# Performance work log

Hardware: AMD Instinct MI355X
Metric: run time of the kernel (lower is better)

Reference implementation:

```python
import jax, jax.numpy as jnp
import numpy as np

N_NODES = 100000
N_EDGES = 1600000
IN_DIM = 128
HID = 128
OUT = 40


def setup_inputs() -> dict:
    key = jax.random.key(0)
    ks = jax.random.split(key, 8)
    x = jax.random.normal(ks[0], (N_NODES, IN_DIM), dtype=jnp.float32)
    edge_index = jax.random.randint(ks[1], (2, N_EDGES), 0, N_NODES, dtype=jnp.int64)
    def glorot(k, fan_in, fan_out):
        s = jnp.sqrt(6.0 / (fan_in + fan_out)).astype(jnp.float32)
        return jax.random.uniform(k, (fan_in, fan_out), jnp.float32, -s, s)
    return {
        "x": x,
        "edge_index": edge_index,
        "W1": glorot(ks[2], IN_DIM, HID), "b1": jnp.zeros((HID,), jnp.float32),
        "W2": glorot(ks[3], HID, HID),    "b2": jnp.zeros((HID,), jnp.float32),
        "W3": glorot(ks[4], HID, HID),    "b3": jnp.zeros((HID,), jnp.float32),
        "Wl": glorot(ks[5], HID, OUT),    "bl": jnp.zeros((OUT,), jnp.float32),
    }


def _gcn_norm(edge_index, num_nodes):
    # PyG GCNConv default: add self-loops, symmetric normalization.
    loops = jnp.arange(num_nodes, dtype=edge_index.dtype)
    src = jnp.concatenate([edge_index[0], loops])
    dst = jnp.concatenate([edge_index[1], loops])
    deg = jax.ops.segment_sum(jnp.ones_like(dst, dtype=jnp.float32), dst,
                              num_segments=num_nodes)
    dis = jnp.where(deg > 0, jax.lax.rsqrt(deg), 0.0)  # deg^{-1/2}
    norm = dis[src] * dis[dst]  # [E+N]
    return src, dst, norm


def _gcn_conv(x, W, b, src, dst, norm, num_nodes):
    h = x @ W                                   # [N, F_out]
    msg = h[src] * norm[:, None]                # gather + scale
    out = jax.ops.segment_sum(msg, dst, num_segments=num_nodes)
    return out + b


def reference(x, edge_index, W1, b1, W2, b2, W3, b3, Wl, bl):
    n = x.shape[0]
    src, dst, norm = _gcn_norm(edge_index, n)
    h = jax.nn.relu(_gcn_conv(x, W1, b1, src, dst, norm, n))
    h = jax.nn.relu(_gcn_conv(h, W2, b2, src, dst, norm, n))
    h = _gcn_conv(h, W3, b3, src, dst, norm, n)
    # dropout p=0.5 is identity in eval mode
    return h @ Wl + bl
```

## Files before the change

kernel.cpp:

```cpp
#include <hip/hip_runtime.h>

typedef __attribute__((ext_vector_type(8))) short sh8;
typedef __attribute__((ext_vector_type(4))) float f4;

__device__ __forceinline__ float bf2f(unsigned short u) {
    union { unsigned int u; float f; } c; c.u = ((unsigned int)u) << 16; return c.f;
}
__device__ __forceinline__ unsigned short f2bf(float f) {
    union { float f; unsigned int u; } c; c.f = f;
    unsigned int x = c.u;
    unsigned int r = (x + 0x7fffu + ((x >> 16) & 1u)) >> 16;
    return (unsigned short)r;
}
__device__ __forceinline__ void bfsplit(float x, short& hi, short& lo) {
    unsigned short h = f2bf(x);
    float r = x - bf2f(h);
    hi = (short)h;
    lo = (short)f2bf(r);
}

__global__ void k_zero_cnt(int* cnt, int N) {
    int i = blockIdx.x * 256 + threadIdx.x;
    if (i < N) cnt[i] = 0;
}

__global__ void k_count(const int* __restrict__ dst, int* __restrict__ cnt, int E, int N) {
    int E4 = E >> 2;
    for (int i = blockIdx.x * 256 + threadIdx.x; i < E4; i += gridDim.x * 256) {
        int4 d = ((const int4*)dst)[i];
        if ((unsigned)d.x < (unsigned)N) atomicAdd(&cnt[d.x], 1);
        if ((unsigned)d.y < (unsigned)N) atomicAdd(&cnt[d.y], 1);
        if ((unsigned)d.z < (unsigned)N) atomicAdd(&cnt[d.z], 1);
        if ((unsigned)d.w < (unsigned)N) atomicAdd(&cnt[d.w], 1);
    }
    if (blockIdx.x == 0) {
        for (int e = (E4 << 2) + threadIdx.x; e < E; e += 256) {
            int d = dst[e];
            if ((unsigned)d < (unsigned)N) atomicAdd(&cnt[d], 1);
        }
    }
}

#define SCAN_B 256
__global__ void k_scan_a(const int* __restrict__ cnt, int* __restrict__ rowptr,
                         int* __restrict__ bsum, float* __restrict__ dis, int N) {
    __shared__ int sh[SCAN_B];
    int t = threadIdx.x, i = blockIdx.x * SCAN_B + t;
    int v = (i < N) ? cnt[i] : 0;
    if (i < N) dis[i] = rsqrtf((float)(v + 1));
    sh[t] = v; __syncthreads();
    for (int off = 1; off < SCAN_B; off <<= 1) {
        int x = (t >= off) ? sh[t - off] : 0;
        __syncthreads();
        sh[t] += x;
        __syncthreads();
    }
    int incl = sh[t];
    if (i < N) rowptr[i] = incl - v;
    if (t == SCAN_B - 1) bsum[blockIdx.x] = incl;
}

__global__ void k_scan_b(int* bsum, int NB) {
    __shared__ int sh[512];
    int t = threadIdx.x;
    int v = (t < NB) ? bsum[t] : 0;
    sh[t] = v; __syncthreads();
    for (int off = 1; off < 512; off <<= 1) {
        int x = (t >= off) ? sh[t - off] : 0;
        __syncthreads();
        sh[t] += x;
        __syncthreads();
    }
    if (t < NB) bsum[t] = sh[t] - v;
}

__global__ void k_scan_c(int* __restrict__ rowptr, int* __restrict__ cursor,
                         const int* __restrict__ bsum, int N) {
    int i = blockIdx.x * 256 + threadIdx.x;
    if (i < N) {
        int r = rowptr[i] + bsum[blockIdx.x];
        rowptr[i] = r;
        cursor[i] = r;
    }
}

__global__ void k_fill(const int* __restrict__ src, const int* __restrict__ dst,
                       int* __restrict__ cursor, int* __restrict__ csrc, int E, int N) {
    int g = blockIdx.x & 7;
    int j = blockIdx.x >> 3;
    int nb = gridDim.x >> 3;
    int lo = (int)((long long)g * N / 8);
    int hi = (int)((long long)(g + 1) * N / 8);
    int E4 = E >> 2;
    for (int i = j * 256 + threadIdx.x; i < E4; i += nb * 256) {
        int4 d4 = ((const int4*)dst)[i];
        int e = i << 2;
        #pragma unroll
        for (int q = 0; q < 4; ++q) {
            int d = (q == 0) ? d4.x : (q == 1) ? d4.y : (q == 2) ? d4.z : d4.w;
            if (d < lo || d >= hi) continue;
            int s = src[e + q];
            if ((unsigned)s >= (unsigned)N) continue;
            int p = atomicAdd(&cursor[d], 1);
            csrc[p] = s;
        }
    }
    if (blockIdx.x == 0) {
        for (int e = (E4 << 2) + threadIdx.x; e < E; e += 256) {
            int d = dst[e];
            int s = src[e];
            if ((unsigned)d >= (unsigned)N || (unsigned)s >= (unsigned)N) continue;
            int p = atomicAdd(&cursor[d], 1);
            csrc[p] = s;
        }
    }
}

__global__ __launch_bounds__(256)
void k_gemm128_a32(const float* __restrict__ X,
                   const float* __restrict__ W,
                   const float* __restrict__ dis,
                   unsigned short* __restrict__ H, int nPairs) {
    int wave = threadIdx.x >> 6;
    int lane = threadIdx.x & 63;
    int ln = lane & 15, quad = lane >> 4;
    int c0 = (wave & 1) * 64;
    int subTile = wave >> 1;

    sh8 bh[4][4], blo[4][4];
    #pragma unroll
    for (int nt = 0; nt < 4; ++nt) {
        int col = c0 + nt * 16 + ln;
        #pragma unroll
        for (int kt = 0; kt < 4; ++kt) {
            int k0 = kt * 32 + quad * 8;
            #pragma unroll
            for (int j = 0; j < 8; ++j) {
                short h, l;
                bfsplit(W[(k0 + j) * 128 + col], h, l);
                bh[nt][kt][j] = h; blo[nt][kt][j] = l;
            }
        }
    }

    for (int p = blockIdx.x; p < nPairs; p += gridDim.x) {
        int nodeBase = p * 32 + subTile * 16;
        const float* xrow = X + (nodeBase + ln) * 128 + quad * 8;
        sh8 ah[4], al[4];
        #pragma unroll
        for (int kt = 0; kt < 4; ++kt) {
            f4 v0 = *(const f4*)(xrow + kt * 32);
            f4 v1 = *(const f4*)(xrow + kt * 32 + 4);
            #pragma unroll
            for (int j = 0; j < 4; ++j) {
                short h, l;
                bfsplit(v0[j], h, l); ah[kt][j] = h; al[kt][j] = l;
                bfsplit(v1[j], h, l); ah[kt][j + 4] = h; al[kt][j + 4] = l;
            }
        }

        f4 acc[4] = { {0.f,0.f,0.f,0.f}, {0.f,0.f,0.f,0.f}, {0.f,0.f,0.f,0.f}, {0.f,0.f,0.f,0.f} };
        #pragma unroll
        for (int kt = 0; kt < 4; ++kt)
            #pragma unroll
            for (int nt = 0; nt < 4; ++nt) {
                acc[nt] = __builtin_amdgcn_mfma_f32_16x16x32_bf16(ah[kt], bh[nt][kt], acc[nt], 0, 0, 0);
                acc[nt] = __builtin_amdgcn_mfma_f32_16x16x32_bf16(ah[kt], blo[nt][kt], acc[nt], 0, 0, 0);
                acc[nt] = __builtin_amdgcn_mfma_f32_16x16x32_bf16(al[kt], bh[nt][kt], acc[nt], 0, 0, 0);
            }

        float ds[4];
        #pragma unroll
        for (int r = 0; r < 4; ++r) ds[r] = dis[nodeBase + quad * 4 + r];
        #pragma unroll
        for (int nt = 0; nt < 4; ++nt) {
            int col = c0 + nt * 16 + ln;
            #pragma unroll
            for (int r = 0; r < 4; ++r)
                H[(nodeBase + quad * 4 + r) * 128 + col] = f2bf(acc[nt][r] * ds[r]);
        }
    }
}

__global__ __launch_bounds__(256)
void k_gemm128_a16(const unsigned short* __restrict__ X,
                   const float* __restrict__ W,
                   const float* __restrict__ dis,
                   unsigned short* __restrict__ H, int nPairs) {
    int wave = threadIdx.x >> 6;
    int lane = threadIdx.x & 63;
    int ln = lane & 15, quad = lane >> 4;
    int c0 = (wave & 1) * 64;
    int subTile = wave >> 1;

    sh8 bh[4][4], blo[4][4];
    #pragma unroll
    for (int nt = 0; nt < 4; ++nt) {
        int col = c0 + nt * 16 + ln;
        #pragma unroll
        for (int kt = 0; kt < 4; ++kt) {
            int k0 = kt * 32 + quad * 8;
            #pragma unroll
            for (int j = 0; j < 8; ++j) {
                short h, l;
                bfsplit(W[(k0 + j) * 128 + col], h, l);
                bh[nt][kt][j] = h; blo[nt][kt][j] = l;
            }
        }
    }

    for (int p = blockIdx.x; p < nPairs; p += gridDim.x) {
        int nodeBase = p * 32 + subTile * 16;
        const unsigned short* xrow = X + (nodeBase + ln) * 128 + quad * 8;
        sh8 a[4];
        #pragma unroll
        for (int kt = 0; kt < 4; ++kt) a[kt] = *(const sh8*)(xrow + kt * 32);

        f4 acc[4] = { {0.f,0.f,0.f,0.f}, {0.f,0.f,0.f,0.f}, {0.f,0.f,0.f,0.f}, {0.f,0.f,0.f,0.f} };
        #pragma unroll
        for (int kt = 0; kt < 4; ++kt)
            #pragma unroll
            for (int nt = 0; nt < 4; ++nt) {
                acc[nt] = __builtin_amdgcn_mfma_f32_16x16x32_bf16(a[kt], bh[nt][kt], acc[nt], 0, 0, 0);
                acc[nt] = __builtin_amdgcn_mfma_f32_16x16x32_bf16(a[kt], blo[nt][kt], acc[nt], 0, 0, 0);
            }

        float ds[4];
        #pragma unroll
        for (int r = 0; r < 4; ++r) ds[r] = dis[nodeBase + quad * 4 + r];
        #pragma unroll
        for (int nt = 0; nt < 4; ++nt) {
            int col = c0 + nt * 16 + ln;
            #pragma unroll
            for (int r = 0; r < 4; ++r)
                H[(nodeBase + quad * 4 + r) * 128 + col] = f2bf(acc[nt][r] * ds[r]);
        }
    }
}

__global__ __launch_bounds__(256)
void k_agg(const unsigned short* __restrict__ H,
           unsigned short* __restrict__ O,
           const float* __restrict__ dis,
           const int* __restrict__ rowptr,
           const int* __restrict__ cnt,
           const int* __restrict__ csrc,
           const float* __restrict__ bias,
           int relu, int N) {
    int n = (blockIdx.x * 256 + threadIdx.x) >> 5;
    if (n >= N) return;
    int lane = threadIdx.x & 31;
    int sub  = lane & 15;
    int half = lane >> 4;

    float a0 = 0.f, a1 = 0.f, a2 = 0.f, a3 = 0.f;
    float a4 = 0.f, a5 = 0.f, a6 = 0.f, a7 = 0.f;

    auto addrow = [&](uint4 v) {
        a0 += bf2f((unsigned short)v.x);
        a1 += bf2f((unsigned short)(v.x >> 16));
        a2 += bf2f((unsigned short)v.y);
        a3 += bf2f((unsigned short)(v.y >> 16));
        a4 += bf2f((unsigned short)v.z);
        a5 += bf2f((unsigned short)(v.z >> 16));
        a6 += bf2f((unsigned short)v.w);
        a7 += bf2f((unsigned short)(v.w >> 16));
    };

    if (half == 0)
        addrow(*(const uint4*)(H + (size_t)n * 128 + sub * 8));

    int start = rowptr[n];
    int e = cnt[n];
    int i = 0;
    for (; i + 8 <= e; i += 8) {
        int s[4];
        #pragma unroll
        for (int q = 0; q < 4; ++q) s[q] = csrc[start + i + 2 * q + half];
        uint4 v[4];
        #pragma unroll
        for (int q = 0; q < 4; ++q) v[q] = *(const uint4*)(H + (size_t)s[q] * 128 + sub * 8);
        #pragma unroll
        for (int q = 0; q < 4; ++q) addrow(v[q]);
    }
    for (int j = i + half; j < e; j += 2) {
        int s = csrc[start + j];
        addrow(*(const uint4*)(H + (size_t)s * 128 + sub * 8));
    }

    a0 += __shfl_xor(a0, 16); a1 += __shfl_xor(a1, 16);
    a2 += __shfl_xor(a2, 16); a3 += __shfl_xor(a3, 16);
    a4 += __shfl_xor(a4, 16); a5 += __shfl_xor(a5, 16);
    a6 += __shfl_xor(a6, 16); a7 += __shfl_xor(a7, 16);

    if (half == 0) {
        float dn = dis[n];
        f4 b0 = *(const f4*)(bias + sub * 8);
        f4 b1 = *(const f4*)(bias + sub * 8 + 4);
        a0 = a0 * dn + b0[0]; a1 = a1 * dn + b0[1];
        a2 = a2 * dn + b0[2]; a3 = a3 * dn + b0[3];
        a4 = a4 * dn + b1[0]; a5 = a5 * dn + b1[1];
        a6 = a6 * dn + b1[2]; a7 = a7 * dn + b1[3];
        if (relu) {
            a0 = fmaxf(a0, 0.f); a1 = fmaxf(a1, 0.f);
            a2 = fmaxf(a2, 0.f); a3 = fmaxf(a3, 0.f);
            a4 = fmaxf(a4, 0.f); a5 = fmaxf(a5, 0.f);
            a6 = fmaxf(a6, 0.f); a7 = fmaxf(a7, 0.f);
        }
        uint4 ov;
        ov.x = (unsigned int)f2bf(a0) | ((unsigned int)f2bf(a1) << 16);
        ov.y = (unsigned int)f2bf(a2) | ((unsigned int)f2bf(a3) << 16);
        ov.z = (unsigned int)f2bf(a4) | ((unsigned int)f2bf(a5) << 16);
        ov.w = (unsigned int)f2bf(a6) | ((unsigned int)f2bf(a7) << 16);
        *(uint4*)(O + (size_t)n * 128 + sub * 8) = ov;
    }
}

__global__ __launch_bounds__(256)
void k_gemm_final(const unsigned short* __restrict__ X,
                  const float* __restrict__ W,
                  const float* __restrict__ bl,
                  float* __restrict__ OUT, int nTiles) {
    int wave = threadIdx.x >> 6;
    int lane = threadIdx.x & 63;
    int ln = lane & 15, quad = lane >> 4;
    int tile = blockIdx.x * 4 + wave;
    if (tile >= nTiles) return;

    sh8 bh[3][4], blo[3][4];
    #pragma unroll
    for (int nt = 0; nt < 3; ++nt) {
        int col = nt * 16 + ln;
        bool valid = (col < 40);
        #pragma unroll
        for (int kt = 0; kt < 4; ++kt) {
            int k0 = kt * 32 + quad * 8;
            #pragma unroll
            for (int j = 0; j < 8; ++j) {
                short h = 0, l = 0;
                if (valid) bfsplit(W[(k0 + j) * 40 + col], h, l);
                bh[nt][kt][j] = h; blo[nt][kt][j] = l;
            }
        }
    }

    int nodeBase = tile * 16;
    const unsigned short* xrow = X + (nodeBase + ln) * 128 + quad * 8;
    sh8 a[4];
    #pragma unroll
    for (int kt = 0; kt < 4; ++kt) a[kt] = *(const sh8*)(xrow + kt * 32);

    f4 acc[3] = { {0.f,0.f,0.f,0.f}, {0.f,0.f,0.f,0.f}, {0.f,0.f,0.f,0.f} };
    #pragma unroll
    for (int kt = 0; kt < 4; ++kt)
        #pragma unroll
        for (int nt = 0; nt < 3; ++nt) {
            acc[nt] = __builtin_amdgcn_mfma_f32_16x16x32_bf16(a[kt], bh[nt][kt], acc[nt], 0, 0, 0);
            acc[nt] = __builtin_amdgcn_mfma_f32_16x16x32_bf16(a[kt], blo[nt][kt], acc[nt], 0, 0, 0);
        }

    #pragma unroll
    for (int nt = 0; nt < 3; ++nt) {
        int col = nt * 16 + ln;
        if (col < 40) {
            float bv = bl[col];
            #pragma unroll
            for (int r = 0; r < 4; ++r)
                OUT[(nodeBase + quad * 4 + r) * 40 + col] = acc[nt][r] + bv;
        }
    }
}

extern "C" void kernel_launch(void* const* d_in, const int* in_sizes, int n_in,
                              void* d_out, int out_size, void* d_ws, size_t ws_size,
                              hipStream_t stream) {
    const float* x  = (const float*)d_in[0];
    const int*   ei = (const int*)d_in[1];
    const float* W1 = (const float*)d_in[2];
    const float* b1 = (const float*)d_in[3];
    const float* W2 = (const float*)d_in[4];
    const float* b2 = (const float*)d_in[5];
    const float* W3 = (const float*)d_in[6];
    const float* b3 = (const float*)d_in[7];
    const float* Wl = (const float*)d_in[8];
    const float* bl = (const float*)d_in[9];

    const int N = in_sizes[0] / 128;
    const int E = in_sizes[1] / 2;
    const int* srcIdx = ei;
    const int* dstIdx = ei + E;

    char* ws = (char*)d_ws;
    size_t off = 0;
    auto alloc = [&](size_t bytes) { void* p = ws + off; off += (bytes + 511) & ~(size_t)511; return p; };
    int*   cnt     = (int*)  alloc((size_t)N * 4);
    int*   rowptr  = (int*)  alloc((size_t)N * 4);
    int*   cursor  = (int*)  alloc((size_t)N * 4);
    float* dis     = (float*)alloc((size_t)N * 4);
    int*   bsum    = (int*)  alloc(512 * 4);
    int*   csrc    = (int*)  alloc((size_t)E * 4);
    unsigned short* h0 = (unsigned short*)alloc((size_t)N * 128 * 2);
    unsigned short* h1 = (unsigned short*)alloc((size_t)N * 128 * 2);

    const int gN = (N + 255) / 256;
    const int nPairs = N / 32;
    const int nTiles = N / 16;
    const int gAgg = (N * 32 + 255) / 256;
    const int gPart = 2048;

    k_zero_cnt<<<gN, 256, 0, stream>>>(cnt, N);
    k_count<<<1568, 256, 0, stream>>>(dstIdx, cnt, E, N);
    k_scan_a<<<gN, 256, 0, stream>>>(cnt, rowptr, bsum, dis, N);
    k_scan_b<<<1, 512, 0, stream>>>(bsum, gN);
    k_scan_c<<<gN, 256, 0, stream>>>(rowptr, cursor, bsum, N);
    k_fill<<<gPart, 256, 0, stream>>>(srcIdx, dstIdx, cursor, csrc, E, N);

    k_gemm128_a32<<<768, 256, 0, stream>>>(x, W1, dis, h0, nPairs);
    k_agg<<<gAgg, 256, 0, stream>>>(h0, h1, dis, rowptr, cnt, csrc, b1, 1, N);
    k_gemm128_a16<<<768, 256, 0, stream>>>(h1, W2, dis, h0, nPairs);
    k_agg<<<gAgg, 256, 0, stream>>>(h0, h1, dis, rowptr, cnt, csrc, b2, 1, N);
    k_gemm128_a16<<<768, 256, 0, stream>>>(h1, W3, dis, h0, nPairs);
    k_agg<<<gAgg, 256, 0, stream>>>(h0, h1, dis, rowptr, cnt, csrc, b3, 0, N);
    k_gemm_final<<<(nTiles + 3) / 4, 256, 0, stream>>>(h1, Wl, bl, (float*)d_out, nTiles);
}
```

Before: 539.1 us.

## Store hidden features in 16-wide feature panels and aggregate per panel

```diff
diff --git a/kernel.cpp b/kernel.cpp
--- a/kernel.cpp
+++ b/kernel.cpp
@@ -2,6 +2,7 @@
 
 typedef __attribute__((ext_vector_type(8))) short sh8;
 typedef __attribute__((ext_vector_type(4))) float f4;
+typedef __attribute__((ext_vector_type(4))) unsigned int u4;
 
 __device__ __forceinline__ float bf2f(unsigned short u) {
     union { unsigned int u; float f; } c; c.u = ((unsigned int)u) << 16; return c.f;
@@ -18,6 +19,7 @@
     hi = (short)h;
     lo = (short)f2bf(r);
 }
+
 
 __global__ void k_zero_cnt(int* cnt, int N) {
     int i = blockIdx.x * 256 + threadIdx.x;
@@ -126,6 +128,7 @@
     int ln = lane & 15, quad = lane >> 4;
     int c0 = (wave & 1) * 64;
     int subTile = wave >> 1;
+    const size_t Nn = (size_t)nPairs * 32;
 
     sh8 bh[4][4], blo[4][4];
     #pragma unroll
@@ -172,12 +175,13 @@
         float ds[4];
         #pragma unroll
         for (int r = 0; r < 4; ++r) ds[r] = dis[nodeBase + quad * 4 + r];
+        int fpan = (wave & 1) * 4;
         #pragma unroll
         for (int nt = 0; nt < 4; ++nt) {
-            int col = c0 + nt * 16 + ln;
+            size_t pb = ((size_t)(fpan + nt) * Nn) * 16;
             #pragma unroll
             for (int r = 0; r < 4; ++r)
-                H[(nodeBase + quad * 4 + r) * 128 + col] = f2bf(acc[nt][r] * ds[r]);
+                H[pb + (size_t)(nodeBase + quad * 4 + r) * 16 + ln] = f2bf(acc[nt][r] * ds[r]);
         }
     }
 }
@@ -192,6 +196,7 @@
     int ln = lane & 15, quad = lane >> 4;
     int c0 = (wave & 1) * 64;
     int subTile = wave >> 1;
+    const size_t Nn = (size_t)nPairs * 32;
 
     sh8 bh[4][4], blo[4][4];
     #pragma unroll
@@ -211,10 +216,14 @@
 
     for (int p = blockIdx.x; p < nPairs; p += gridDim.x) {
         int nodeBase = p * 32 + subTile * 16;
-        const unsigned short* xrow = X + (nodeBase + ln) * 128 + quad * 8;
         sh8 a[4];
         #pragma unroll
-        for (int kt = 0; kt < 4; ++kt) a[kt] = *(const sh8*)(xrow + kt * 32);
+        for (int kt = 0; kt < 4; ++kt) {
+            int feat0 = kt * 32 + quad * 8;
+            const unsigned short* ap =
+                X + ((size_t)(feat0 >> 4) * Nn + (nodeBase + ln)) * 16 + (feat0 & 15);
+            a[kt] = *(const sh8*)ap;
+        }
 
         f4 acc[4] = { {0.f,0.f,0.f,0.f}, {0.f,0.f,0.f,0.f}, {0.f,0.f,0.f,0.f}, {0.f,0.f,0.f,0.f} };
         #pragma unroll
@@ -228,12 +237,13 @@
         float ds[4];
         #pragma unroll
         for (int r = 0; r < 4; ++r) ds[r] = dis[nodeBase + quad * 4 + r];
+        int fpan = (wave & 1) * 4;
         #pragma unroll
         for (int nt = 0; nt < 4; ++nt) {
-            int col = c0 + nt * 16 + ln;
+            size_t pb = ((size_t)(fpan + nt) * Nn) * 16;
             #pragma unroll
             for (int r = 0; r < 4; ++r)
-                H[(nodeBase + quad * 4 + r) * 128 + col] = f2bf(acc[nt][r] * ds[r]);
+                H[pb + (size_t)(nodeBase + quad * 4 + r) * 16 + ln] = f2bf(acc[nt][r] * ds[r]);
         }
     }
 }
@@ -247,16 +257,30 @@
            const int* __restrict__ csrc,
            const float* __restrict__ bias,
            int relu, int N) {
-    int n = (blockIdx.x * 256 + threadIdx.x) >> 5;
+    int f = blockIdx.x & 7;
+    int chunk = blockIdx.x >> 3;
+    int pairIdx = threadIdx.x >> 1;
+    int h = threadIdx.x & 1;
+    int n = chunk * 128 + pairIdx;
     if (n >= N) return;
-    int lane = threadIdx.x & 31;
-    int sub  = lane & 15;
-    int half = lane >> 4;
-
-    float a0 = 0.f, a1 = 0.f, a2 = 0.f, a3 = 0.f;
-    float a4 = 0.f, a5 = 0.f, a6 = 0.f, a7 = 0.f;
-
-    auto addrow = [&](uint4 v) {
+
+    const unsigned short* P = H + ((size_t)f * N) * 16;
+    unsigned short*       Q = O + ((size_t)f * N) * 16;
+
+    float a0, a1, a2, a3, a4, a5, a6, a7;
+    {
+        u4 v = *(const u4*)(P + (size_t)n * 16 + h * 8);
+        a0 = bf2f((unsigned short)v.x);
+        a1 = bf2f((unsigned short)(v.x >> 16));
+        a2 = bf2f((unsigned short)v.y);
+        a3 = bf2f((unsigned short)(v.y >> 16));
+        a4 = bf2f((unsigned short)v.z);
+        a5 = bf2f((unsigned short)(v.z >> 16));
+        a6 = bf2f((unsigned short)v.w);
+        a7 = bf2f((unsigned short)(v.w >> 16));
+    }
+
+    auto addrow = [&](u4 v) {
         a0 += bf2f((unsigned short)v.x);
         a1 += bf2f((unsigned short)(v.x >> 16));
         a2 += bf2f((unsigned short)v.y);
@@ -267,53 +291,43 @@
         a7 += bf2f((unsigned short)(v.w >> 16));
     };
 
-    if (half == 0)
-        addrow(*(const uint4*)(H + (size_t)n * 128 + sub * 8));
-
     int start = rowptr[n];
     int e = cnt[n];
     int i = 0;
     for (; i + 8 <= e; i += 8) {
-        int s[4];
-        #pragma unroll
-        for (int q = 0; q < 4; ++q) s[q] = csrc[start + i + 2 * q + half];
-        uint4 v[4];
-        #pragma unroll
-        for (int q = 0; q < 4; ++q) v[q] = *(const uint4*)(H + (size_t)s[q] * 128 + sub * 8);
-        #pragma unroll
-        for (int q = 0; q < 4; ++q) addrow(v[q]);
-    }
-    for (int j = i + half; j < e; j += 2) {
-        int s = csrc[start + j];
-        addrow(*(const uint4*)(H + (size_t)s * 128 + sub * 8));
-    }
-
-    a0 += __shfl_xor(a0, 16); a1 += __shfl_xor(a1, 16);
-    a2 += __shfl_xor(a2, 16); a3 += __shfl_xor(a3, 16);
-    a4 += __shfl_xor(a4, 16); a5 += __shfl_xor(a5, 16);
-    a6 += __shfl_xor(a6, 16); a7 += __shfl_xor(a7, 16);
-
-    if (half == 0) {
-        float dn = dis[n];
-        f4 b0 = *(const f4*)(bias + sub * 8);
-        f4 b1 = *(const f4*)(bias + sub * 8 + 4);
-        a0 = a0 * dn + b0[0]; a1 = a1 * dn + b0[1];
-        a2 = a2 * dn + b0[2]; a3 = a3 * dn + b0[3];
-        a4 = a4 * dn + b1[0]; a5 = a5 * dn + b1[1];
-        a6 = a6 * dn + b1[2]; a7 = a7 * dn + b1[3];
-        if (relu) {
-            a0 = fmaxf(a0, 0.f); a1 = fmaxf(a1, 0.f);
-            a2 = fmaxf(a2, 0.f); a3 = fmaxf(a3, 0.f);
-            a4 = fmaxf(a4, 0.f); a5 = fmaxf(a5, 0.f);
-            a6 = fmaxf(a6, 0.f); a7 = fmaxf(a7, 0.f);
-        }
-        uint4 ov;
-        ov.x = (unsigned int)f2bf(a0) | ((unsigned int)f2bf(a1) << 16);
-        ov.y = (unsigned int)f2bf(a2) | ((unsigned int)f2bf(a3) << 16);
-        ov.z = (unsigned int)f2bf(a4) | ((unsigned int)f2bf(a5) << 16);
-        ov.w = (unsigned int)f2bf(a6) | ((unsigned int)f2bf(a7) << 16);
-        *(uint4*)(O + (size_t)n * 128 + sub * 8) = ov;
-    }
+        int s[8];
+        #pragma unroll
+        for (int q = 0; q < 8; ++q) s[q] = __builtin_nontemporal_load(&csrc[start + i + q]);
+        u4 v[8];
+        #pragma unroll
+        for (int q = 0; q < 8; ++q) v[q] = *(const u4*)(P + (size_t)s[q] * 16 + h * 8);
+        #pragma unroll
+        for (int q = 0; q < 8; ++q) addrow(v[q]);
+    }
+    for (; i < e; ++i) {
+        int s = __builtin_nontemporal_load(&csrc[start + i]);
+        addrow(*(const u4*)(P + (size_t)s * 16 + h * 8));
+    }
+
+    float dn = dis[n];
+    f4 b0 = *(const f4*)(bias + f * 16 + h * 8);
+    f4 b1 = *(const f4*)(bias + f * 16 + h * 8 + 4);
+    a0 = a0 * dn + b0[0]; a1 = a1 * dn + b0[1];
+    a2 = a2 * dn + b0[2]; a3 = a3 * dn + b0[3];
+    a4 = a4 * dn + b1[0]; a5 = a5 * dn + b1[1];
+    a6 = a6 * dn + b1[2]; a7 = a7 * dn + b1[3];
+    if (relu) {
+        a0 = fmaxf(a0, 0.f); a1 = fmaxf(a1, 0.f);
+        a2 = fmaxf(a2, 0.f); a3 = fmaxf(a3, 0.f);
+        a4 = fmaxf(a4, 0.f); a5 = fmaxf(a5, 0.f);
+        a6 = fmaxf(a6, 0.f); a7 = fmaxf(a7, 0.f);
+    }
+    u4 ov;
+    ov.x = (unsigned int)f2bf(a0) | ((unsigned int)f2bf(a1) << 16);
+    ov.y = (unsigned int)f2bf(a2) | ((unsigned int)f2bf(a3) << 16);
+    ov.z = (unsigned int)f2bf(a4) | ((unsigned int)f2bf(a5) << 16);
+    ov.w = (unsigned int)f2bf(a6) | ((unsigned int)f2bf(a7) << 16);
+    __builtin_nontemporal_store(ov, (u4*)(Q + (size_t)n * 16 + h * 8));
 }
 
 __global__ __launch_bounds__(256)
@@ -326,6 +340,7 @@
     int ln = lane & 15, quad = lane >> 4;
     int tile = blockIdx.x * 4 + wave;
     if (tile >= nTiles) return;
+    const size_t Nn = (size_t)nTiles * 16;
 
     sh8 bh[3][4], blo[3][4];
     #pragma unroll
@@ -345,10 +360,14 @@
     }
 
     int nodeBase = tile * 16;
-    const unsigned short* xrow = X + (nodeBase + ln) * 128 + quad * 8;
     sh8 a[4];
     #pragma unroll
-    for (int kt = 0; kt < 4; ++kt) a[kt] = *(const sh8*)(xrow + kt * 32);
+    for (int kt = 0; kt < 4; ++kt) {
+        int feat0 = kt * 32 + quad * 8;
+        const unsigned short* ap =
+            X + ((size_t)(feat0 >> 4) * Nn + (nodeBase + ln)) * 16 + (feat0 & 15);
+        a[kt] = *(const sh8*)ap;
+    }
 
     f4 acc[3] = { {0.f,0.f,0.f,0.f}, {0.f,0.f,0.f,0.f}, {0.f,0.f,0.f,0.f} };
     #pragma unroll
@@ -405,7 +424,7 @@
     const int gN = (N + 255) / 256;
     const int nPairs = N / 32;
     const int nTiles = N / 16;
-    const int gAgg = (N * 32 + 255) / 256;
+    const int gAgg = 8 * ((N + 127) / 128);
     const int gPart = 2048;
 
     k_zero_cnt<<<gN, 256, 0, stream>>>(cnt, N);
```

Result: slower. 768.2 us (+42.5%).

## Merge CSR fill and first-layer GEMM into one launch

Applied to the files above, without the earlier changes.

```diff
diff --git a/kernel.cpp b/kernel.cpp
--- a/kernel.cpp
+++ b/kernel.cpp
@@ -84,11 +84,17 @@
     }
 }
 
-__global__ void k_fill(const int* __restrict__ src, const int* __restrict__ dst,
-                       int* __restrict__ cursor, int* __restrict__ csrc, int E, int N) {
-    int g = blockIdx.x & 7;
-    int j = blockIdx.x >> 3;
-    int nb = gridDim.x >> 3;
+#define FILL_BLOCKS 2048
+#define GEMM1_BLOCKS 768
+
+__device__ __forceinline__ void fill_body(const int* __restrict__ src,
+                                          const int* __restrict__ dst,
+                                          int* __restrict__ cursor,
+                                          int* __restrict__ csrc, int E, int N) {
+    int bid = blockIdx.x;
+    int g = bid & 7;
+    int j = bid >> 3;
+    int nb = FILL_BLOCKS >> 3;
     int lo = (int)((long long)g * N / 8);
     int hi = (int)((long long)(g + 1) * N / 8);
     int E4 = E >> 2;
@@ -105,7 +111,7 @@
             csrc[p] = s;
         }
     }
-    if (blockIdx.x == 0) {
+    if (bid == 0) {
         for (int e = (E4 << 2) + threadIdx.x; e < E; e += 256) {
             int d = dst[e];
             int s = src[e];
@@ -116,11 +122,11 @@
     }
 }
 
-__global__ __launch_bounds__(256)
-void k_gemm128_a32(const float* __restrict__ X,
-                   const float* __restrict__ W,
-                   const float* __restrict__ dis,
-                   unsigned short* __restrict__ H, int nPairs) {
+__device__ __forceinline__ void gemm1_body(const float* __restrict__ X,
+                                           const float* __restrict__ W,
+                                           const float* __restrict__ dis,
+                                           unsigned short* __restrict__ H, int nPairs) {
+    int bid = blockIdx.x - FILL_BLOCKS;
     int wave = threadIdx.x >> 6;
     int lane = threadIdx.x & 63;
     int ln = lane & 15, quad = lane >> 4;
@@ -143,7 +149,7 @@
         }
     }
 
-    for (int p = blockIdx.x; p < nPairs; p += gridDim.x) {
+    for (int p = bid; p < nPairs; p += GEMM1_BLOCKS) {
         int nodeBase = p * 32 + subTile * 16;
         const float* xrow = X + (nodeBase + ln) * 128 + quad * 8;
         sh8 ah[4], al[4];
@@ -180,6 +186,18 @@
                 H[(nodeBase + quad * 4 + r) * 128 + col] = f2bf(acc[nt][r] * ds[r]);
         }
     }
+}
+
+__global__ __launch_bounds__(256)
+void k_fill_gemm1(const int* __restrict__ src, const int* __restrict__ dst,
+                  int* __restrict__ cursor, int* __restrict__ csrc, int E, int N,
+                  const float* __restrict__ X, const float* __restrict__ W,
+                  const float* __restrict__ dis, unsigned short* __restrict__ H,
+                  int nPairs) {
+    if (blockIdx.x < FILL_BLOCKS)
+        fill_body(src, dst, cursor, csrc, E, N);
+    else
+        gemm1_body(X, W, dis, H, nPairs);
 }
 
 __global__ __launch_bounds__(256)
@@ -406,16 +424,16 @@
     const int nPairs = N / 32;
     const int nTiles = N / 16;
     const int gAgg = (N * 32 + 255) / 256;
-    const int gPart = 2048;
 
     k_zero_cnt<<<gN, 256, 0, stream>>>(cnt, N);
     k_count<<<1568, 256, 0, stream>>>(dstIdx, cnt, E, N);
     k_scan_a<<<gN, 256, 0, stream>>>(cnt, rowptr, bsum, dis, N);
     k_scan_b<<<1, 512, 0, stream>>>(bsum, gN);
     k_scan_c<<<gN, 256, 0, stream>>>(rowptr, cursor, bsum, N);
-    k_fill<<<gPart, 256, 0, stream>>>(srcIdx, dstIdx, cursor, csrc, E, N);
-
-    k_gemm128_a32<<<768, 256, 0, stream>>>(x, W1, dis, h0, nPairs);
+
+    k_fill_gemm1<<<FILL_BLOCKS + GEMM1_BLOCKS, 256, 0, stream>>>(
+        srcIdx, dstIdx, cursor, csrc, E, N, x, W1, dis, h0, nPairs);
+
     k_agg<<<gAgg, 256, 0, stream>>>(h0, h1, dis, rowptr, cnt, csrc, b1, 1, N);
     k_gemm128_a16<<<768, 256, 0, stream>>>(h1, W2, dis, h0, nPairs);
     k_agg<<<gAgg, 256, 0, stream>>>(h0, h1, dis, rowptr, cnt, csrc, b2, 1, N);
```

Result: slower. 618.4 us (+14.7%).

## Record per-edge rank during degree counting to build CSR without fill atomics

Applied to the files above, without the earlier changes.

```diff
diff --git a/kernel.cpp b/kernel.cpp
--- a/kernel.cpp
+++ b/kernel.cpp
@@ -24,19 +24,22 @@
     if (i < N) cnt[i] = 0;
 }
 
-__global__ void k_count(const int* __restrict__ dst, int* __restrict__ cnt, int E, int N) {
+__global__ void k_count(const int* __restrict__ dst, int* __restrict__ cnt,
+                        int* __restrict__ rank, int E, int N) {
     int E4 = E >> 2;
     for (int i = blockIdx.x * 256 + threadIdx.x; i < E4; i += gridDim.x * 256) {
         int4 d = ((const int4*)dst)[i];
-        if ((unsigned)d.x < (unsigned)N) atomicAdd(&cnt[d.x], 1);
-        if ((unsigned)d.y < (unsigned)N) atomicAdd(&cnt[d.y], 1);
-        if ((unsigned)d.z < (unsigned)N) atomicAdd(&cnt[d.z], 1);
-        if ((unsigned)d.w < (unsigned)N) atomicAdd(&cnt[d.w], 1);
+        int4 r;
+        r.x = ((unsigned)d.x < (unsigned)N) ? atomicAdd(&cnt[d.x], 1) : -1;
+        r.y = ((unsigned)d.y < (unsigned)N) ? atomicAdd(&cnt[d.y], 1) : -1;
+        r.z = ((unsigned)d.z < (unsigned)N) ? atomicAdd(&cnt[d.z], 1) : -1;
+        r.w = ((unsigned)d.w < (unsigned)N) ? atomicAdd(&cnt[d.w], 1) : -1;
+        ((int4*)rank)[i] = r;
     }
     if (blockIdx.x == 0) {
         for (int e = (E4 << 2) + threadIdx.x; e < E; e += 256) {
             int d = dst[e];
-            if ((unsigned)d < (unsigned)N) atomicAdd(&cnt[d], 1);
+            rank[e] = ((unsigned)d < (unsigned)N) ? atomicAdd(&cnt[d], 1) : -1;
         }
     }
 }
@@ -74,44 +77,35 @@
     if (t < NB) bsum[t] = sh[t] - v;
 }
 
-__global__ void k_scan_c(int* __restrict__ rowptr, int* __restrict__ cursor,
-                         const int* __restrict__ bsum, int N) {
+__global__ void k_scan_c(int* __restrict__ rowptr, const int* __restrict__ bsum, int N) {
     int i = blockIdx.x * 256 + threadIdx.x;
-    if (i < N) {
-        int r = rowptr[i] + bsum[blockIdx.x];
-        rowptr[i] = r;
-        cursor[i] = r;
-    }
+    if (i < N) rowptr[i] += bsum[blockIdx.x];
 }
 
 __global__ void k_fill(const int* __restrict__ src, const int* __restrict__ dst,
-                       int* __restrict__ cursor, int* __restrict__ csrc, int E, int N) {
-    int g = blockIdx.x & 7;
-    int j = blockIdx.x >> 3;
-    int nb = gridDim.x >> 3;
-    int lo = (int)((long long)g * N / 8);
-    int hi = (int)((long long)(g + 1) * N / 8);
+                       const int* __restrict__ rank, const int* __restrict__ rowptr,
+                       int* __restrict__ csrc, int E, int N) {
     int E4 = E >> 2;
-    for (int i = j * 256 + threadIdx.x; i < E4; i += nb * 256) {
+    for (int i = blockIdx.x * 256 + threadIdx.x; i < E4; i += gridDim.x * 256) {
         int4 d4 = ((const int4*)dst)[i];
-        int e = i << 2;
+        int4 s4 = ((const int4*)src)[i];
+        int4 r4 = ((const int4*)rank)[i];
         #pragma unroll
         for (int q = 0; q < 4; ++q) {
             int d = (q == 0) ? d4.x : (q == 1) ? d4.y : (q == 2) ? d4.z : d4.w;
-            if (d < lo || d >= hi) continue;
-            int s = src[e + q];
-            if ((unsigned)s >= (unsigned)N) continue;
-            int p = atomicAdd(&cursor[d], 1);
-            csrc[p] = s;
+            int s = (q == 0) ? s4.x : (q == 1) ? s4.y : (q == 2) ? s4.z : s4.w;
+            int r = (q == 0) ? r4.x : (q == 1) ? r4.y : (q == 2) ? r4.z : r4.w;
+            if ((unsigned)d >= (unsigned)N || (unsigned)s >= (unsigned)N || r < 0) continue;
+            csrc[rowptr[d] + r] = s;
         }
     }
     if (blockIdx.x == 0) {
         for (int e = (E4 << 2) + threadIdx.x; e < E; e += 256) {
             int d = dst[e];
             int s = src[e];
-            if ((unsigned)d >= (unsigned)N || (unsigned)s >= (unsigned)N) continue;
-            int p = atomicAdd(&cursor[d], 1);
-            csrc[p] = s;
+            int r = rank[e];
+            if ((unsigned)d >= (unsigned)N || (unsigned)s >= (unsigned)N || r < 0) continue;
+            csrc[rowptr[d] + r] = s;
         }
     }
 }
@@ -395,25 +389,24 @@
     auto alloc = [&](size_t bytes) { void* p = ws + off; off += (bytes + 511) & ~(size_t)511; return p; };
     int*   cnt     = (int*)  alloc((size_t)N * 4);
     int*   rowptr  = (int*)  alloc((size_t)N * 4);
-    int*   cursor  = (int*)  alloc((size_t)N * 4);
     float* dis     = (float*)alloc((size_t)N * 4);
     int*   bsum    = (int*)  alloc(512 * 4);
     int*   csrc    = (int*)  alloc((size_t)E * 4);
     unsigned short* h0 = (unsigned short*)alloc((size_t)N * 128 * 2);
     unsigned short* h1 = (unsigned short*)alloc((size_t)N * 128 * 2);
+    int* rank = (int*)h0;
 
     const int gN = (N + 255) / 256;
     const int nPairs = N / 32;
     const int nTiles = N / 16;
     const int gAgg = (N * 32 + 255) / 256;
-    const int gPart = 2048;
 
     k_zero_cnt<<<gN, 256, 0, stream>>>(cnt, N);
-    k_count<<<1568, 256, 0, stream>>>(dstIdx, cnt, E, N);
+    k_count<<<1568, 256, 0, stream>>>(dstIdx, cnt, rank, E, N);
     k_scan_a<<<gN, 256, 0, stream>>>(cnt, rowptr, bsum, dis, N);
     k_scan_b<<<1, 512, 0, stream>>>(bsum, gN);
-    k_scan_c<<<gN, 256, 0, stream>>>(rowptr, cursor, bsum, N);
-    k_fill<<<gPart, 256, 0, stream>>>(srcIdx, dstIdx, cursor, csrc, E, N);
+    k_scan_c<<<gN, 256, 0, stream>>>(rowptr, bsum, N);
+    k_fill<<<1568, 256, 0, stream>>>(srcIdx, dstIdx, rank, rowptr, csrc, E, N);
 
     k_gemm128_a32<<<768, 256, 0, stream>>>(x, W1, dis, h0, nPairs);
     k_agg<<<gAgg, 256, 0, stream>>>(h0, h1, dis, rowptr, cnt, csrc, b1, 1, N);
```

Measured after the change: 492.1 us. -8.7%, faster.
